# Kernel tuning notes

Measured on AMD Instinct MI355X. Metric: run time of the kernel, lower is better.

The kernel has to match this reference:

```python
import jax, jax.numpy as jnp
import numpy as np

B, T, D, H, O = 256, 256, 128, 1024, 64


def setup_inputs() -> dict:
    key = jax.random.key(0)
    ks = jax.random.split(key, 24)
    std = 0.02
    x = jax.random.normal(ks[0], (B, T, D), jnp.float32)
    delta = jax.random.uniform(ks[1], (B, T, D), jnp.float32) * 5.0  # positive time gaps
    m = (jax.random.uniform(ks[2], (B, T, D)) < 0.8).astype(jnp.float32)  # {0,1} mask
    p = lambda i, shp: jax.random.normal(ks[i], shp, jnp.float32) * std
    return {
        'x': x, 'delta': delta, 'm': m,
        'W_r': p(3, (D, H)), 'U_r': p(4, (H, H)), 'V_r': p(5, (D, H)), 'b_r': jnp.zeros((H,), jnp.float32),
        'W_z': p(6, (D, H)), 'U_z': p(7, (H, H)), 'V_z': p(8, (D, H)), 'b_z': jnp.zeros((H,), jnp.float32),
        'W':   p(9, (D, H)), 'U':   p(10, (H, H)), 'V':  p(11, (D, H)), 'b':  jnp.zeros((H,), jnp.float32),
        'W_gamma_x': p(12, (D,)), 'b_gamma_x': jnp.zeros((D,), jnp.float32),
        'W_gamma_h': p(13, (D, H)), 'b_gamma_h': jnp.zeros((H,), jnp.float32),
        'dec_W': p(14, (H, O)), 'dec_b': jnp.zeros((O,), jnp.float32),
    }


def _grud_forward(x, delta, m, W_r, U_r, V_r, b_r, W_z, U_z, V_z, b_z,
                  W, U, V, b, W_gamma_x, b_gamma_x, W_gamma_h, b_gamma_h, dec_W, dec_b):
    # input decay (per-feature affine on delta); X_last_obs buffer is zeros
    decay_x = delta * W_gamma_x + b_gamma_x                      # [B,T,D]
    x_replace = (1.0 - decay_x) * 0.001                          # decay_x * 0 + (1-decay_x)*0.001
    x = jnp.where(m > 0, x_replace, x)                           # x[m.byte()] = x_replace[m.byte()]
    # hidden decay gates, precomputed for all t
    gamma_h = jnp.exp(-jnp.maximum(0.0, jnp.einsum('btd,dh->bth', m, W_gamma_h) + b_gamma_h))
    mi = 1.0 - m
    # precompute all input-side projections (batched GEMMs outside the scan)
    pre_z = jnp.einsum('btd,dh->bth', x, W_z) + jnp.einsum('btd,dh->bth', mi, V_z) + b_z
    pre_r = jnp.einsum('btd,dh->bth', x, W_r) + jnp.einsum('btd,dh->bth', mi, V_r) + b_r
    pre_h = jnp.einsum('btd,dh->bth', x, W) + jnp.einsum('btd,dh->bth', mi, V) + b

    def step(h, inp):
        pz, pr, ph, gh = inp                                     # each [B,H]
        h = gh * h
        z = jax.nn.sigmoid(pz + h @ U_z)
        r = jax.nn.sigmoid(pr + h @ U_r)
        h_tilde = jnp.tanh(ph + (r * h) @ U)
        h = (1.0 - z) * h + z * h_tilde
        return h, None

    h0 = jnp.zeros((x.shape[0], U.shape[0]), x.dtype)
    seq = (jnp.swapaxes(pre_z, 0, 1), jnp.swapaxes(pre_r, 0, 1),
           jnp.swapaxes(pre_h, 0, 1), jnp.swapaxes(gamma_h, 0, 1))
    h_T, _ = jax.lax.scan(step, h0, seq)
    # eval mode: dropout masks are all-ones, decoder_dropout identity, bn at init is ~identity
    out = h_T @ dec_W + dec_b                                    # [B,O]
    return out


def reference(x, delta, m, W_r, U_r, V_r, b_r, W_z, U_z, V_z, b_z,
              W, U, V, b, W_gamma_x, b_gamma_x, W_gamma_h, b_gamma_h, dec_W, dec_b):
    return _grud_forward(x, delta, m, W_r, U_r, V_r, b_r, W_z, U_z, V_z, b_z,
                         W, U, V, b, W_gamma_x, b_gamma_x, W_gamma_h, b_gamma_h, dec_W, dec_b)
```

## Files before the change

kernel.cpp:

```cpp
#include <hip/hip_runtime.h>
#include <hip/hip_bf16.h>

using short8v = __attribute__((ext_vector_type(8))) short;
using float4v = __attribute__((ext_vector_type(4))) float;
typedef unsigned int uint32;

#define MFMA_B16(a,b,c) __builtin_amdgcn_mfma_f32_16x16x32_bf16((a),(b),(c),0,0,0)

constexpr int Bc = 256, Tc = 256, Dc = 128, Hc = 1024;
constexpr int KB_L = 19;
constexpr int KB_V = 12;
constexpr int KB_S = 9;

constexpr size_t OFF_FA   = 0;
constexpr size_t OFF_FB   = 1024;
constexpr size_t OFF_HDEC = 4096;
constexpr size_t OFF_RH   = OFF_HDEC + 524288;
constexpr size_t OFF_HT   = OFF_RH + 524288;
constexpr size_t OFF_XM   = 4u << 20;
constexpr size_t OFF_WL   = OFF_XM + 33554432;
constexpr size_t OFF_WV   = OFF_WL + 3735552;
constexpr size_t OFF_WS   = OFF_WV + 2359296;
constexpr size_t OFF_WG   = OFF_WS + 1769472;
constexpr size_t OFF_BIAS = OFF_WG + 262144;
constexpr size_t OFF_BG   = OFF_BIAS + 12288;

constexpr int LO_WL   = 0;
constexpr int LO_ACH0 = 116736;
constexpr int LO_ACH1 = 133120;
constexpr int LO_ZBUF = 149504;
constexpr int LO_GBUF = 153728;
constexpr int LO_HBUF = 157952;
constexpr int LO_BIAS = 160064;
constexpr int LO_BG   = 160448;
constexpr int SMEM_BYTES = 160576;

typedef __attribute__((address_space(1))) const unsigned int g_as1_u32;
typedef __attribute__((address_space(3))) unsigned int l_as3_u32;

__device__ __forceinline__ unsigned short f2bf(float f) {
  __hip_bfloat16 h = __float2bfloat16(f);
  return *reinterpret_cast<unsigned short*>(&h);
}
__device__ __forceinline__ float bf2f(unsigned short s) {
  return __uint_as_float(((unsigned int)s) << 16);
}

#define BARX() asm volatile("s_waitcnt lgkmcnt(0)\n\ts_barrier" ::: "memory")
#define WAITV2() asm volatile("s_waitcnt vmcnt(2)" ::: "memory")
#define WAITV0() asm volatile("s_waitcnt vmcnt(0)" ::: "memory")

__global__ void k_init(char* __restrict__ ws) {
  int id = blockIdx.x * 256 + threadIdx.x;
  if (id < 132096) {
    uint32* p = (uint32*)ws + id;
    __hip_atomic_store(p, 0u, __ATOMIC_RELAXED, __HIP_MEMORY_SCOPE_AGENT);
  }
}

__global__ void k_xm(const float* __restrict__ x, const float* __restrict__ delta,
                     const float* __restrict__ m, const float* __restrict__ wgx,
                     const float* __restrict__ bgx, unsigned short* __restrict__ xm) {
  const int eid = blockIdx.x * 256 + threadIdx.x;
  const int d = eid & 127; const int bt = eid >> 7;
  const int t = bt >> 8;   const int b = bt & 255;
  const size_t ii = ((size_t)b * Tc + t) * Dc + d;
  const float xv = x[ii], dv = delta[ii], mv = m[ii];
  const float dx = dv * wgx[d] + bgx[d];
  const float xo = (mv > 0.f) ? (1.f - dx) * 0.001f : xv;
  const size_t o = ((size_t)t * Bc + b) * 256;
  xm[o + d] = f2bf(xo);
  xm[o + 128 + d] = f2bf(mv);
}

__global__ void k_pack(const float* __restrict__ Wz, const float* __restrict__ Uz,
                       const float* __restrict__ Vz, const float* __restrict__ bz,
                       const float* __restrict__ Wr, const float* __restrict__ Ur,
                       const float* __restrict__ Vr, const float* __restrict__ br,
                       const float* __restrict__ Wh, const float* __restrict__ Uh,
                       const float* __restrict__ Vh, const float* __restrict__ bh,
                       const float* __restrict__ Wgh, const float* __restrict__ bgh,
                       char* __restrict__ ws) {
  unsigned short* wL = (unsigned short*)(ws + OFF_WL);
  unsigned short* wV = (unsigned short*)(ws + OFF_WV);
  unsigned short* wS = (unsigned short*)(ws + OFF_WS);
  unsigned short* wG = (unsigned short*)(ws + OFF_WG);
  float* bias = (float*)(ws + OFF_BIAS);
  float* bg   = (float*)(ws + OFF_BG);
  const int id = blockIdx.x * 256 + threadIdx.x;
  if (id < 491520) {
    const int l = id & 63; int u = id >> 6;
    const int kb = u % 40; u /= 40;
    const int tile = u % 6; const int mem = u / 6;
    const int role = tile >> 1;
    const float* Wm = role == 0 ? Wz : (role == 1 ? Wr : Wh);
    const float* Vm = role == 0 ? Vz : (role == 1 ? Vr : Vh);
    const float* Um = role == 0 ? Uz : (role == 1 ? Ur : Uh);
    const int col = mem * 32 + (tile & 1) * 16 + (l & 15);
    const int k0 = kb * 32 + (l >> 4) * 8;
    unsigned short* dst;
    if (kb < KB_L)
      dst = wL + ((((size_t)mem * 6 + tile) * KB_L + kb) * 64 + l) * 8;
    else if (kb < KB_L + KB_V)
      dst = wV + ((((size_t)mem * 6 + tile) * KB_V + (kb - KB_L)) * 64 + l) * 8;
    else
      dst = wS + ((((size_t)mem * 6 + tile) * KB_S + (kb - KB_L - KB_V)) * 64 + l) * 8;
    #pragma unroll
    for (int e = 0; e < 8; ++e) {
      const int k = k0 + e; float v;
      if (k < 128)      v =  Wm[(size_t)k * Hc + col];
      else if (k < 256) v = -Vm[(size_t)(k - 128) * Hc + col];
      else              v =  Um[(size_t)(k - 256) * Hc + col];
      dst[e] = f2bf(v);
    }
  } else if (id < 507904) {
    const int id2 = id - 491520;
    const int l = id2 & 63; int u = id2 >> 6;
    const int kb = u & 3; u >>= 2;
    const int tile = u & 1; const int mem = u >> 1;
    const int col = mem * 32 + tile * 16 + (l & 15);
    const int k0 = kb * 32 + (l >> 4) * 8;
    unsigned short* dst = wG + ((((size_t)mem * 2 + tile) * 4 + kb) * 64 + l) * 8;
    #pragma unroll
    for (int e = 0; e < 8; ++e) dst[e] = f2bf(Wgh[(size_t)(k0 + e) * Hc + col]);
  } else if (id < 510976) {
    const int id3 = id - 507904;
    const int c16 = id3 & 15; int u = id3 >> 4;
    const int tile = u % 6; const int mem = u / 6;
    const int role = tile >> 1;
    const float* Vm = role == 0 ? Vz : (role == 1 ? Vr : Vh);
    const float* bm = role == 0 ? bz : (role == 1 ? br : bh);
    const int col = mem * 32 + (tile & 1) * 16 + c16;
    float s = bm[col];
    for (int d = 0; d < 128; ++d) s += Vm[(size_t)d * Hc + col];
    bias[mem * 96 + tile * 16 + c16] = s;
  } else if (id < 512000) {
    bg[id - 510976] = bgh[id - 510976];
  }
}

__device__ __forceinline__ void issue_chunk(const unsigned short* gsrc, int colbase,
                                            char* achbuf, int w, int lane) {
  #pragma unroll
  for (int j = 0; j < 2; ++j) {
    const int seg  = w * 2 + j;
    const int rrow = seg * 2 + (lane >> 5);
    const unsigned inrow = (unsigned)((lane & 31) * 16);
    const unsigned goff  = inrow ^ (unsigned)((rrow & 7) * 64);
    const unsigned char* gp = (const unsigned char*)(gsrc + (size_t)rrow * Hc + colbase) + goff;
    __builtin_amdgcn_global_load_lds((g_as1_u32*)gp, (l_as3_u32*)(achbuf + seg * 1024),
                                     16, 0,  0x11);
  }
}

template<int S>
__device__ __forceinline__ void mfma_slot(const short* achb, int afr, int swiz,
                                          const short* wlrl, const short8v (&vw)[2][KB_V],
                                          const short* wsrl, float4v& a0, float4v& a1) {
  #pragma unroll
  for (int kk = 0; kk < 8; ++kk) {
    const int kb = S * 8 + kk;
    short8v av = *(const short8v*)(achb + afr + ((kk * 32) ^ swiz));
    short8v b0, b1;
    if (kb < KB_L) {
      b0 = *(const short8v*)(wlrl + (0 * KB_L + kb) * 512);
      b1 = *(const short8v*)(wlrl + (1 * KB_L + kb) * 512);
    } else if (kb < KB_L + KB_V) {
      b0 = vw[0][kb - KB_L]; b1 = vw[1][kb - KB_L];
    } else {
      b0 = *(const short8v*)(wsrl + (0 * KB_S + (kb - KB_L - KB_V)) * 512);
      b1 = *(const short8v*)(wsrl + (1 * KB_S + (kb - KB_L - KB_V)) * 512);
    }
    a0 = MFMA_B16(av, b0, a0);
    a1 = MFMA_B16(av, b1, a1);
  }
}

__device__ __forceinline__ void store_row32(unsigned short* gbase, int rowq, int mem,
                                            int l15, int q4, unsigned short v0,
                                            unsigned short v1) {
  int s1 = q4 * 16 + ((2 * l15) & 15);
  int a0 = __shfl((int)v0, s1), a1 = __shfl((int)v1, s1);
  unsigned lo = (l15 < 8) ? (unsigned)a0 : (unsigned)a1;
  int s2 = q4 * 16 + ((2 * l15 + 1) & 15);
  int b0 = __shfl((int)v0, s2), b1 = __shfl((int)v1, s2);
  unsigned hi = (l15 < 8) ? (unsigned)b0 : (unsigned)b1;
  unsigned pk = (lo & 0xffffu) | (hi << 16);
  uint32* p = (uint32*)gbase + (size_t)rowq * (Hc / 2) + mem * 16 + l15;
  __hip_atomic_store(p, pk, __ATOMIC_RELAXED, __HIP_MEMORY_SCOPE_AGENT);
}

__device__ __forceinline__ void poll_ge(int* flags, int tval, int l) {
  int sp = 0;
  while (true) {
    int v = (l < 32) ? __hip_atomic_load(&flags[l], __ATOMIC_RELAXED, __HIP_MEMORY_SCOPE_AGENT)
                     : 0x7fffffff;
    if (__all(v >= tval)) break;
    if (++sp > (1 << 16)) break;
    __builtin_amdgcn_s_sleep(1);
  }
}

__global__ __launch_bounds__(512, 2) void k_grud(const unsigned short* __restrict__ xm,
                                                 char* __restrict__ ws) {
  extern __shared__ char smem[];
  short* wLl  = (short*)(smem + LO_WL);
  char*  ach0 = smem + LO_ACH0;
  char*  ach1 = smem + LO_ACH1;
  float* zbuf = (float*)(smem + LO_ZBUF);
  float* gbuf = (float*)(smem + LO_GBUF);
  unsigned short* hbuf = (unsigned short*)(smem + LO_HBUF);
  float* biasl = (float*)(smem + LO_BIAS);
  float* bgl   = (float*)(smem + LO_BG);

  const int bid = blockIdx.x, g = bid & 7, mem = bid >> 3;
  const int tid = threadIdx.x, w = tid >> 6, l = tid & 63;
  const int l15 = l & 15, q4 = l >> 4;
  const int role3 = (w >> 1) < 3 ? (w >> 1) : 2;
  const int mt = w & 1;
  const int row = mt * 16 + l15;
  const int afr = row * 256 + q4 * 8;
  const int swiz = (row & 7) * 32;

  int* fA = (int*)(ws + OFF_FA) + g * 32;
  int* fB = (int*)(ws + OFF_FB) + g * 32;
  unsigned short* hdec = (unsigned short*)(ws + OFF_HDEC) + (size_t)g * 32 * Hc;
  unsigned short* rhb  = (unsigned short*)(ws + OFF_RH)  + (size_t)g * 32 * Hc;
  float* hT = (float*)(ws + OFF_HT);
  const short* wLg = (const short*)(ws + OFF_WL) + (size_t)mem * (6 * KB_L * 512);
  const short* wVg = (const short*)(ws + OFF_WV) + (size_t)mem * (6 * KB_V * 512);
  const short* wSg = (const short*)(ws + OFF_WS) + (size_t)mem * (6 * KB_S * 512);
  const short* wGl = (const short*)(ws + OFF_WG) + (size_t)mem * (2 * 4 * 512) + l * 8;
  const float* biasg = (const float*)(ws + OFF_BIAS) + mem * 96;
  const float* bgg   = (const float*)(ws + OFF_BG) + mem * 32;

  for (int i = tid; i < 6 * KB_L * 512 / 8; i += 512) ((uint4*)wLl)[i] = ((const uint4*)wLg)[i];
  if (tid < 96) biasl[tid] = biasg[tid];
  if (tid < 32) bgl[tid] = bgg[tid];
  for (int i = tid; i < 1056; i += 512) hbuf[i] = 0;

  short8v vw[2][KB_V];
  #pragma unroll
  for (int c = 0; c < 2; ++c)
    #pragma unroll
    for (int i = 0; i < KB_V; ++i)
      vw[c][i] = *(const short8v*)(wVg + (size_t)(((role3 * 2 + c) * KB_V + i) * 512 + l * 8));

  const short* wlrl = wLl + role3 * (2 * KB_L * 512) + l * 8;
  const short* wsrl = wSg + role3 * (2 * KB_S * 512) + l * 8;
  __syncthreads();

  float4v acc0, acc1;
  #pragma unroll 1
  for (int t = 0; t < 256; ++t) {
    const unsigned short* xmt = xm + ((size_t)t * Bc + g * 32) * 256;
    if (w < 6) {
      acc0 = float4v{0.f, 0.f, 0.f, 0.f};
      acc1 = float4v{0.f, 0.f, 0.f, 0.f};
      const unsigned short* xr = xmt + (size_t)row * 256 + q4 * 8;
      #pragma unroll
      for (int kk = 0; kk < 8; ++kk) {
        short8v av = *(const short8v*)(xr + kk * 32);
        short8v b0 = *(const short8v*)(wlrl + (0 * KB_L + kk) * 512);
        short8v b1 = *(const short8v*)(wlrl + (1 * KB_L + kk) * 512);
        acc0 = MFMA_B16(av, b0, acc0);
        acc1 = MFMA_B16(av, b1, acc1);
      }
    } else if (t < 255) {
      float4v ga0{0.f, 0.f, 0.f, 0.f}, ga1{0.f, 0.f, 0.f, 0.f};
      const unsigned short* mr = xmt + (size_t)Bc * 256 + (size_t)row * 256 + 128 + q4 * 8;
      #pragma unroll
      for (int kb = 0; kb < 4; ++kb) {
        short8v av = *(const short8v*)(mr + kb * 32);
        short8v b0 = *(const short8v*)(wGl + (0 * 4 + kb) * 512);
        short8v b1 = *(const short8v*)(wGl + (1 * 4 + kb) * 512);
        ga0 = MFMA_B16(av, b0, ga0);
        ga1 = MFMA_B16(av, b1, ga1);
      }
      #pragma unroll
      for (int q = 0; q < 4; ++q) {
        const int rq = mt * 16 + q4 * 4 + q;
        gbuf[l15 * 33 + rq]        = __expf(-fmaxf(0.f, ga0[q] + bgl[l15]));
        gbuf[(16 + l15) * 33 + rq] = __expf(-fmaxf(0.f, ga1[q] + bgl[16 + l15]));
      }
    }
    if (w == 7) poll_ge(fB, t, l);
    BARX();
    issue_chunk(hdec, 0,   ach0, w, l);
    issue_chunk(hdec, 256, ach1, w, l);
    WAITV2(); BARX();
    if (w < 4) mfma_slot<1>((short*)ach0, afr, swiz, wlrl, vw, wsrl, acc0, acc1);
    BARX();
    issue_chunk(hdec, 512, ach0, w, l);
    WAITV2(); BARX();
    if (w < 4) mfma_slot<2>((short*)ach1, afr, swiz, wlrl, vw, wsrl, acc0, acc1);
    BARX();
    issue_chunk(hdec, 768, ach1, w, l);
    WAITV2(); BARX();
    if (w < 4) mfma_slot<3>((short*)ach0, afr, swiz, wlrl, vw, wsrl, acc0, acc1);
    BARX();
    WAITV0(); BARX();
    if (w < 4) mfma_slot<4>((short*)ach1, afr, swiz, wlrl, vw, wsrl, acc0, acc1);
    if (w < 2) {
      #pragma unroll
      for (int c = 0; c < 2; ++c) {
        float4v a = c ? acc1 : acc0;
        #pragma unroll
        for (int q = 0; q < 4; ++q) {
          const int rq = mt * 16 + q4 * 4 + q;
          zbuf[(c * 16 + l15) * 33 + rq] = 1.f / (1.f + __expf(-(a[q] + biasl[c * 16 + l15])));
        }
      }
    } else if (w < 4) {
      #pragma unroll
      for (int q = 0; q < 4; ++q) {
        const int rq = mt * 16 + q4 * 4 + q;
        unsigned short u0, u1;
        #pragma unroll
        for (int c = 0; c < 2; ++c) {
          float4v a = c ? acc1 : acc0;
          const float rv = 1.f / (1.f + __expf(-(a[q] + biasl[32 + c * 16 + l15])));
          const float hd = bf2f(hbuf[(c * 16 + l15) * 33 + rq]);
          unsigned short pv = f2bf(rv * hd);
          if (c == 0) u0 = pv; else u1 = pv;
        }
        store_row32(rhb, rq, mem, l15, q4, u0, u1);
      }
      WAITV0();
    }
    BARX();
    if (tid == 0) __hip_atomic_store(&fA[mem], t + 1, __ATOMIC_RELAXED, __HIP_MEMORY_SCOPE_AGENT);
    if (w == 7) poll_ge(fA, t + 1, l);
    BARX();
    issue_chunk(rhb, 0,   ach0, w, l);
    issue_chunk(rhb, 256, ach1, w, l);
    WAITV2(); BARX();
    if (w == 4 || w == 5) mfma_slot<1>((short*)ach0, afr, swiz, wlrl, vw, wsrl, acc0, acc1);
    BARX();
    issue_chunk(rhb, 512, ach0, w, l);
    WAITV2(); BARX();
    if (w == 4 || w == 5) mfma_slot<2>((short*)ach1, afr, swiz, wlrl, vw, wsrl, acc0, acc1);
    BARX();
    issue_chunk(rhb, 768, ach1, w, l);
    WAITV2(); BARX();
    if (w == 4 || w == 5) mfma_slot<3>((short*)ach0, afr, swiz, wlrl, vw, wsrl, acc0, acc1);
    BARX();
    WAITV0(); BARX();
    if (w == 4 || w == 5) mfma_slot<4>((short*)ach1, afr, swiz, wlrl, vw, wsrl, acc0, acc1);
    if (w == 4 || w == 5) {
      #pragma unroll
      for (int q = 0; q < 4; ++q) {
        const int rq = mt * 16 + q4 * 4 + q;
        unsigned short u0 = 0, u1 = 0;
        #pragma unroll
        for (int c = 0; c < 2; ++c) {
          float4v a = c ? acc1 : acc0;
          const int cc = c * 16 + l15;
          const float e = __expf(2.f * (a[q] + biasl[64 + cc]));
          const float ht = 1.f - 2.f / (e + 1.f);
          const float zv = zbuf[cc * 33 + rq];
          const float hd = bf2f(hbuf[cc * 33 + rq]);
          const float hn = (1.f - zv) * hd + zv * ht;
          if (t < 255) {
            unsigned short pv = f2bf(gbuf[cc * 33 + rq] * hn);
            hbuf[cc * 33 + rq] = pv;
            if (c == 0) u0 = pv; else u1 = pv;
          } else {
            hT[(size_t)(g * 32 + rq) * Hc + (mem * 32 + cc)] = hn;
          }
        }
        if (t < 255) store_row32(hdec, rq, mem, l15, q4, u0, u1);
      }
      WAITV0();
    }
    BARX();
    if (tid == 0) __hip_atomic_store(&fB[mem], t + 1, __ATOMIC_RELAXED, __HIP_MEMORY_SCOPE_AGENT);
  }
}

__global__ void k_dec(const char* __restrict__ ws, const float* __restrict__ decW,
                      const float* __restrict__ decb, float* __restrict__ out) {
  const float* hT = (const float*)(ws + OFF_HT);
  __shared__ float red[4][64];
  const int b = blockIdx.x, tid = threadIdx.x;
  const int col = tid & 63, part = tid >> 6;
  float acc = 0.f;
  const float* hrow = hT + (size_t)b * Hc + part * 256;
  for (int i = 0; i < 256; ++i) acc += hrow[i] * decW[(size_t)(part * 256 + i) * 64 + col];
  red[part][col] = acc;
  __syncthreads();
  if (part == 0) out[b * 64 + col] = red[0][col] + red[1][col] + red[2][col] + red[3][col] + decb[col];
}

extern "C" void kernel_launch(void* const* d_in, const int* in_sizes, int n_in,
                              void* d_out, int out_size, void* d_ws, size_t ws_size,
                              hipStream_t stream) {
  const float* x    = (const float*)d_in[0];
  const float* delt = (const float*)d_in[1];
  const float* m    = (const float*)d_in[2];
  const float* W_r = (const float*)d_in[3],  *U_r = (const float*)d_in[4];
  const float* V_r = (const float*)d_in[5],  *b_r = (const float*)d_in[6];
  const float* W_z = (const float*)d_in[7],  *U_z = (const float*)d_in[8];
  const float* V_z = (const float*)d_in[9],  *b_z = (const float*)d_in[10];
  const float* W_h = (const float*)d_in[11], *U_h = (const float*)d_in[12];
  const float* V_h = (const float*)d_in[13], *b_h = (const float*)d_in[14];
  const float* Wgx = (const float*)d_in[15], *bgx = (const float*)d_in[16];
  const float* Wgh = (const float*)d_in[17], *bgh = (const float*)d_in[18];
  const float* dW  = (const float*)d_in[19], *db  = (const float*)d_in[20];
  char* ws = (char*)d_ws;
  float* out = (float*)d_out;

  (void)hipFuncSetAttribute((const void*)k_grud,
                            hipFuncAttributeMaxDynamicSharedMemorySize, SMEM_BYTES);

  k_init<<<516, 256, 0, stream>>>(ws);
  k_xm<<<32768, 256, 0, stream>>>(x, delt, m, Wgx, bgx, (unsigned short*)(ws + OFF_XM));
  k_pack<<<2000, 256, 0, stream>>>(W_z, U_z, V_z, b_z, W_r, U_r, V_r, b_r,
                                   W_h, U_h, V_h, b_h, Wgh, bgh, ws);
  k_grud<<<256, 512, SMEM_BYTES, stream>>>((const unsigned short*)(ws + OFF_XM), ws);
  k_dec<<<256, 256, 0, stream>>>(ws, dW, db, out);
}
```

Before: 3.900 ms.

## Stage full hidden-state slab in one shot and rebalance weight residency tiers

Replaces the four-chunk double-buffered load/MFMA pipeline with a single full 32x1024 bf16 load of the hidden state into LDS per phase, followed by one MFMA loop over all K blocks. This cuts the number of barriers per recurrent step. The weight split also changes: fewer K blocks are kept in LDS, more in registers, and slightly fewer are streamed. Launch bounds drop to one block per CU to free registers. The cost is that load latency is no longer overlapped with MFMA work, along with higher register pressure.

```diff
diff --git a/kernel.cpp b/kernel.cpp
--- a/kernel.cpp
+++ b/kernel.cpp
@@ -8,9 +8,9 @@
 #define MFMA_B16(a,b,c) __builtin_amdgcn_mfma_f32_16x16x32_bf16((a),(b),(c),0,0,0)
 
 constexpr int Bc = 256, Tc = 256, Dc = 128, Hc = 1024;
-constexpr int KB_L = 19;
-constexpr int KB_V = 12;
-constexpr int KB_S = 9;
+constexpr int KB_L = 12;
+constexpr int KB_V = 20;
+constexpr int KB_S = 8;
 
 constexpr size_t OFF_FA   = 0;
 constexpr size_t OFF_FB   = 1024;
@@ -19,21 +19,20 @@
 constexpr size_t OFF_HT   = OFF_RH + 524288;
 constexpr size_t OFF_XM   = 4u << 20;
 constexpr size_t OFF_WL   = OFF_XM + 33554432;
-constexpr size_t OFF_WV   = OFF_WL + 3735552;
-constexpr size_t OFF_WS   = OFF_WV + 2359296;
-constexpr size_t OFF_WG   = OFF_WS + 1769472;
+constexpr size_t OFF_WV   = OFF_WL + 2359296;
+constexpr size_t OFF_WS   = OFF_WV + 3932160;
+constexpr size_t OFF_WG   = OFF_WS + 1572864;
 constexpr size_t OFF_BIAS = OFF_WG + 262144;
 constexpr size_t OFF_BG   = OFF_BIAS + 12288;
 
 constexpr int LO_WL   = 0;
-constexpr int LO_ACH0 = 116736;
-constexpr int LO_ACH1 = 133120;
-constexpr int LO_ZBUF = 149504;
-constexpr int LO_GBUF = 153728;
-constexpr int LO_HBUF = 157952;
-constexpr int LO_BIAS = 160064;
-constexpr int LO_BG   = 160448;
-constexpr int SMEM_BYTES = 160576;
+constexpr int LO_PAY  = 73728;
+constexpr int LO_ZBUF = 139264;
+constexpr int LO_GBUF = 143488;
+constexpr int LO_HBUF = 147712;
+constexpr int LO_BIAS = 149824;
+constexpr int LO_BG   = 150208;
+constexpr int SMEM_BYTES = 150336;
 
 typedef __attribute__((address_space(1))) const unsigned int g_as1_u32;
 typedef __attribute__((address_space(3))) unsigned int l_as3_u32;
@@ -47,7 +46,6 @@
 }
 
 #define BARX() asm volatile("s_waitcnt lgkmcnt(0)\n\ts_barrier" ::: "memory")
-#define WAITV2() asm volatile("s_waitcnt vmcnt(2)" ::: "memory")
 #define WAITV0() asm volatile("s_waitcnt vmcnt(0)" ::: "memory")
 
 __global__ void k_init(char* __restrict__ ws) {
@@ -139,28 +137,25 @@
   }
 }
 
-__device__ __forceinline__ void issue_chunk(const unsigned short* gsrc, int colbase,
-                                            char* achbuf, int w, int lane) {
+__device__ __forceinline__ void stage_full(const unsigned short* gsrc, char* buf,
+                                           int w, int l) {
   #pragma unroll
-  for (int j = 0; j < 2; ++j) {
-    const int seg  = w * 2 + j;
-    const int rrow = seg * 2 + (lane >> 5);
-    const unsigned inrow = (unsigned)((lane & 31) * 16);
-    const unsigned goff  = inrow ^ (unsigned)((rrow & 7) * 64);
-    const unsigned char* gp = (const unsigned char*)(gsrc + (size_t)rrow * Hc + colbase) + goff;
-    __builtin_amdgcn_global_load_lds((g_as1_u32*)gp, (l_as3_u32*)(achbuf + seg * 1024),
+  for (int j = 0; j < 8; ++j) {
+    const int seg = w * 8 + j;
+    const int row = seg >> 1;
+    const unsigned off = (unsigned)(((seg & 1) * 1024 + l * 16) ^ ((row & 7) * 16));
+    const unsigned char* gp = (const unsigned char*)(gsrc + (size_t)row * Hc) + off;
+    __builtin_amdgcn_global_load_lds((g_as1_u32*)gp, (l_as3_u32*)(buf + seg * 1024),
                                      16, 0,  0x11);
   }
 }
 
-template<int S>
-__device__ __forceinline__ void mfma_slot(const short* achb, int afr, int swiz,
-                                          const short* wlrl, const short8v (&vw)[2][KB_V],
-                                          const short* wsrl, float4v& a0, float4v& a1) {
+__device__ __forceinline__ void mfma_phase(const char* abase, unsigned aoff, unsigned amask,
+                                           const short* wlrl, const short8v (&vw)[2][KB_V],
+                                           const short* wsrl, float4v& a0, float4v& a1) {
   #pragma unroll
-  for (int kk = 0; kk < 8; ++kk) {
-    const int kb = S * 8 + kk;
-    short8v av = *(const short8v*)(achb + afr + ((kk * 32) ^ swiz));
+  for (int kb = 8; kb < 40; ++kb) {
+    short8v av = *(const short8v*)(abase + (((unsigned)((kb - 8) * 64) + aoff) ^ amask));
     short8v b0, b1;
     if (kb < KB_L) {
       b0 = *(const short8v*)(wlrl + (0 * KB_L + kb) * 512);
@@ -201,12 +196,11 @@
   }
 }
 
-__global__ __launch_bounds__(512, 2) void k_grud(const unsigned short* __restrict__ xm,
+__global__ __launch_bounds__(512, 1) void k_grud(const unsigned short* __restrict__ xm,
                                                  char* __restrict__ ws) {
   extern __shared__ char smem[];
   short* wLl  = (short*)(smem + LO_WL);
-  char*  ach0 = smem + LO_ACH0;
-  char*  ach1 = smem + LO_ACH1;
+  char*  pay  = smem + LO_PAY;
   float* zbuf = (float*)(smem + LO_ZBUF);
   float* gbuf = (float*)(smem + LO_GBUF);
   unsigned short* hbuf = (unsigned short*)(smem + LO_HBUF);
@@ -219,8 +213,9 @@
   const int role3 = (w >> 1) < 3 ? (w >> 1) : 2;
   const int mt = w & 1;
   const int row = mt * 16 + l15;
-  const int afr = row * 256 + q4 * 8;
-  const int swiz = (row & 7) * 32;
+  const char* abase = pay + row * 2048;
+  const unsigned aoff = (unsigned)(q4 * 16);
+  const unsigned amask = (unsigned)((row & 7) * 16);
 
   int* fA = (int*)(ws + OFF_FA) + g * 32;
   int* fB = (int*)(ws + OFF_FB) + g * 32;
@@ -286,21 +281,9 @@
     }
     if (w == 7) poll_ge(fB, t, l);
     BARX();
-    issue_chunk(hdec, 0,   ach0, w, l);
-    issue_chunk(hdec, 256, ach1, w, l);
-    WAITV2(); BARX();
-    if (w < 4) mfma_slot<1>((short*)ach0, afr, swiz, wlrl, vw, wsrl, acc0, acc1);
-    BARX();
-    issue_chunk(hdec, 512, ach0, w, l);
-    WAITV2(); BARX();
-    if (w < 4) mfma_slot<2>((short*)ach1, afr, swiz, wlrl, vw, wsrl, acc0, acc1);
-    BARX();
-    issue_chunk(hdec, 768, ach1, w, l);
-    WAITV2(); BARX();
-    if (w < 4) mfma_slot<3>((short*)ach0, afr, swiz, wlrl, vw, wsrl, acc0, acc1);
-    BARX();
+    stage_full(hdec, pay, w, l);
     WAITV0(); BARX();
-    if (w < 4) mfma_slot<4>((short*)ach1, afr, swiz, wlrl, vw, wsrl, acc0, acc1);
+    if (w < 4) mfma_phase(abase, aoff, amask, wlrl, vw, wsrl, acc0, acc1);
     if (w < 2) {
       #pragma unroll
       for (int c = 0; c < 2; ++c) {
@@ -332,22 +315,10 @@
     if (tid == 0) __hip_atomic_store(&fA[mem], t + 1, __ATOMIC_RELAXED, __HIP_MEMORY_SCOPE_AGENT);
     if (w == 7) poll_ge(fA, t + 1, l);
     BARX();
-    issue_chunk(rhb, 0,   ach0, w, l);
-    issue_chunk(rhb, 256, ach1, w, l);
-    WAITV2(); BARX();
-    if (w == 4 || w == 5) mfma_slot<1>((short*)ach0, afr, swiz, wlrl, vw, wsrl, acc0, acc1);
-    BARX();
-    issue_chunk(rhb, 512, ach0, w, l);
-    WAITV2(); BARX();
-    if (w == 4 || w == 5) mfma_slot<2>((short*)ach1, afr, swiz, wlrl, vw, wsrl, acc0, acc1);
-    BARX();
-    issue_chunk(rhb, 768, ach1, w, l);
-    WAITV2(); BARX();
-    if (w == 4 || w == 5) mfma_slot<3>((short*)ach0, afr, swiz, wlrl, vw, wsrl, acc0, acc1);
-    BARX();
+    stage_full(rhb, pay, w, l);
     WAITV0(); BARX();
-    if (w == 4 || w == 5) mfma_slot<4>((short*)ach1, afr, swiz, wlrl, vw, wsrl, acc0, acc1);
     if (w == 4 || w == 5) {
+      mfma_phase(abase, aoff, amask, wlrl, vw, wsrl, acc0, acc1);
       #pragma unroll
       for (int q = 0; q < 4; ++q) {
         const int rq = mt * 16 + q4 * 4 + q;
```

Result: slower. 7.737 ms (+98.4%).
